# Kernel tuning notes

Hardware: AMD Instinct MI355X
Metric: run time of the kernel (lower is better)

## Reference

```python
import jax, jax.numpy as jnp
import numpy as np

N = 16      # degrees of freedom (state dim = 2N)
HID = 512   # MLP hidden width
B = 2048    # batch


def setup_inputs() -> dict:
    key = jax.random.key(0)
    ks = jax.random.split(key, 4)
    s = 0.05  # small init keeps the qd-qd Hessian block well conditioned
    return {
        "x": jax.random.normal(ks[0], (B, 2 * N), jnp.float32),
        "W1": jax.random.normal(ks[1], (2 * N, HID), jnp.float32) * s,
        "b1": jnp.zeros((HID,), jnp.float32),
        "W2": jax.random.normal(ks[2], (HID, HID), jnp.float32) * s,
        "b2": jnp.zeros((HID,), jnp.float32),
        "W3": jax.random.normal(ks[3], (HID, 1), jnp.float32) * s,
        "b3": jnp.zeros((1,), jnp.float32),
    }


def _lagrangian(qqd, W1, b1, W2, b2, W3, b3):
    # scalar Lagrangian L(q, qd) from a smooth MLP
    h = jax.nn.softplus(qqd @ W1 + b1)
    h = jax.nn.softplus(h @ W2 + b2)
    return (h @ W3 + b3)[0]


def reference(x, W1, b1, W2, b2, W3, b3):
    n = x.shape[1] // 2

    def dyn(qqd):  # qqd: [2n]
        lag = lambda z: _lagrangian(z, W1, b1, W2, b2, W3, b3)
        g = jax.grad(lag)(qqd)                 # J = dL/dqqd, [2n]
        H = jax.jacfwd(jax.grad(lag))(qqd)     # full Hessian, [2n, 2n]
        DL_q = g[:n]                           # dL/dq
        # T_k = sum_j qd_j * d2L/(dq_j dqd_k)  (mixed block)
        T = qqd[n:] @ H[:n, n:]
        Hinv = jnp.linalg.inv(H[n:, n:])       # [n, n], symmetric
        # torch einsum('ijk,ij->ik', inv, v) -> qdd_k = sum_j inv[j,k] v_j
        qdd = (DL_q - T) @ Hinv
        return jnp.concatenate([qqd[n:], qdd])  # [2n] = [qd, qdd]

    return jax.vmap(dyn)(x)
```

## Files before the change

kernel.cpp:

```cpp
#include <hip/hip_runtime.h>
#include <math.h>

#define HID 512
#define TW 32
#define NQ 16

#define SWZM(c) ((((c) + ((c) >> 2) + ((c) >> 4))) & 3)

#define RED6(v) { v += __shfl_xor(v, 32); v += __shfl_xor(v, 16); \
                  v += __shfl_xor(v, 8);  v += __shfl_xor(v, 4);  \
                  v += __shfl_xor(v, 2);  v += __shfl_xor(v, 1); }

__global__ __launch_bounds__(512) void k1_fwd(const float* __restrict__ x,
        const float* __restrict__ W1, const float* __restrict__ b1,
        float* __restrict__ s1g, float* __restrict__ h1g) {
    __shared__ float xr[TW];
    const int r = blockIdx.x;
    const int t = threadIdx.x;
    if (t < TW) xr[t] = x[r * TW + t];
    __syncthreads();
    float z = b1[t];
    #pragma unroll
    for (int k = 0; k < TW; ++k) z = fmaf(xr[k], W1[k * HID + t], z);
    float s = 1.f / (1.f + expf(-z));
    float h = fmaxf(z, 0.f) + log1pf(expf(-fabsf(z)));
    s1g[r * HID + t] = s;
    h1g[r * HID + t] = h;
}

__global__ __launch_bounds__(256) void k2_z2(const float* __restrict__ h1g,
        const float* __restrict__ W2, const float* __restrict__ b2,
        const float* __restrict__ W3,
        float* __restrict__ u2g, float* __restrict__ d2g) {
    __shared__ float As[16 * 36];
    __shared__ float Bs[16 * 64];
    const int tid = threadIdx.x;
    const int r0 = blockIdx.x * 32;
    const int n0 = blockIdx.y * 64;
    const int tm = tid >> 5;
    const int tn = tid & 31;
    float acc[4][2] = {};
    const int ar = tid >> 3;
    const int ak = (tid & 7) * 2;
    const int bk = tid >> 4;
    const int bn = (tid & 15) * 4;
    for (int k0 = 0; k0 < HID; k0 += 16) {
        __syncthreads();
        float2 av = *(const float2*)&h1g[(r0 + ar) * HID + k0 + ak];
        As[(ak + 0) * 36 + ar] = av.x;
        As[(ak + 1) * 36 + ar] = av.y;
        float4 bv = *(const float4*)&W2[(k0 + bk) * HID + n0 + bn];
        *(float4*)&Bs[bk * 64 + bn] = bv;
        __syncthreads();
        #pragma unroll
        for (int k = 0; k < 16; ++k) {
            float4 a4 = *(const float4*)&As[k * 36 + tm * 4];
            float2 bb = *(const float2*)&Bs[k * 64 + tn * 2];
            acc[0][0] = fmaf(a4.x, bb.x, acc[0][0]);
            acc[0][1] = fmaf(a4.x, bb.y, acc[0][1]);
            acc[1][0] = fmaf(a4.y, bb.x, acc[1][0]);
            acc[1][1] = fmaf(a4.y, bb.y, acc[1][1]);
            acc[2][0] = fmaf(a4.z, bb.x, acc[2][0]);
            acc[2][1] = fmaf(a4.z, bb.y, acc[2][1]);
            acc[3][0] = fmaf(a4.w, bb.x, acc[3][0]);
            acc[3][1] = fmaf(a4.w, bb.y, acc[3][1]);
        }
    }
    #pragma unroll
    for (int q = 0; q < 4; ++q) {
        #pragma unroll
        for (int p = 0; p < 2; ++p) {
            int rr = r0 + tm * 4 + q;
            int nn = n0 + tn * 2 + p;
            float z = acc[q][p] + b2[nn];
            float s = 1.f / (1.f + expf(-z));
            float w3v = W3[nn];
            u2g[rr * HID + nn] = s * w3v;
            d2g[rr * HID + nn] = s * (1.f - s) * w3v;
        }
    }
}

__global__ __launch_bounds__(256) void k3_v(const float* __restrict__ u2g,
        const float* __restrict__ W2, float* __restrict__ vg) {
    __shared__ float As[16 * 36];
    __shared__ float Bs[16 * 68];
    const int tid = threadIdx.x;
    const int r0 = blockIdx.x * 32;
    const int n0 = blockIdx.y * 64;
    const int tm = tid >> 5;
    const int tn = tid & 31;
    float acc[4][2] = {};
    const int ar = tid >> 3;
    const int ak = (tid & 7) * 2;
    const int ba = tid >> 2;
    const int bb0 = (tid & 3) * 4;
    for (int k0 = 0; k0 < HID; k0 += 16) {
        __syncthreads();
        float2 av = *(const float2*)&u2g[(r0 + ar) * HID + k0 + ak];
        As[(ak + 0) * 36 + ar] = av.x;
        As[(ak + 1) * 36 + ar] = av.y;
        float4 bv = *(const float4*)&W2[(n0 + ba) * HID + k0 + bb0];
        Bs[(bb0 + 0) * 68 + ba] = bv.x;
        Bs[(bb0 + 1) * 68 + ba] = bv.y;
        Bs[(bb0 + 2) * 68 + ba] = bv.z;
        Bs[(bb0 + 3) * 68 + ba] = bv.w;
        __syncthreads();
        #pragma unroll
        for (int k = 0; k < 16; ++k) {
            float4 a4 = *(const float4*)&As[k * 36 + tm * 4];
            float2 bb = *(const float2*)&Bs[k * 68 + tn * 2];
            acc[0][0] = fmaf(a4.x, bb.x, acc[0][0]);
            acc[0][1] = fmaf(a4.x, bb.y, acc[0][1]);
            acc[1][0] = fmaf(a4.y, bb.x, acc[1][0]);
            acc[1][1] = fmaf(a4.y, bb.y, acc[1][1]);
            acc[2][0] = fmaf(a4.z, bb.x, acc[2][0]);
            acc[2][1] = fmaf(a4.z, bb.y, acc[2][1]);
            acc[3][0] = fmaf(a4.w, bb.x, acc[3][0]);
            acc[3][1] = fmaf(a4.w, bb.y, acc[3][1]);
        }
    }
    #pragma unroll
    for (int q = 0; q < 4; ++q) {
        #pragma unroll
        for (int p = 0; p < 2; ++p) {
            vg[(r0 + tm * 4 + q) * HID + n0 + tn * 2 + p] = acc[q][p];
        }
    }
}

__global__ __launch_bounds__(512) void k2b_pack(const float* __restrict__ x,
        const float* __restrict__ W1, const float* __restrict__ s1g,
        float* __restrict__ s4g, float* __restrict__ u4g,
        float* __restrict__ wt2g) {
    __shared__ float qd[16];
    const int r = blockIdx.x;
    const int c = threadIdx.x;
    if (c < 16) qd[c] = x[r * TW + 16 + c];
    __syncthreads();
    float qw = 0.f;
    #pragma unroll
    for (int m = 0; m < 16; ++m) qw = fmaf(qd[m], W1[m * HID + c], qw);
    const float s = s1g[r * HID + c];
    const int base = (r >> 2) * 2048 + c * 4 + (r & 3);
    s4g[base] = s;
    u4g[base] = s * qw;
    if (r == 0) {
        #pragma unroll
        for (int j = 0; j < 16; ++j)
            wt2g[c * 16 + j] = W1[(16 + j) * HID + c];
    }
}

#define OFF_PT   0
#define OFF_W1T2 8192
#define OFF_WX   16384
#define OFF_YW   17408
#define OFF_H2B  18432
#define OFF_XR   19520
#define OFF_G16  19648
#define OFF_RSB  19712
#define OFF_MU   19776
#define OFF_QD   19840
#define OFF_PIV  19904
#define SMEM_FLOATS 19908

#define ACC16(rr, t)                                   \
  acc[rr][ 0]=fmaf(a0.x,t,acc[rr][ 0]);                \
  acc[rr][ 1]=fmaf(a0.y,t,acc[rr][ 1]);                \
  acc[rr][ 2]=fmaf(a0.z,t,acc[rr][ 2]);                \
  acc[rr][ 3]=fmaf(a0.w,t,acc[rr][ 3]);                \
  acc[rr][ 4]=fmaf(a1.x,t,acc[rr][ 4]);                \
  acc[rr][ 5]=fmaf(a1.y,t,acc[rr][ 5]);                \
  acc[rr][ 6]=fmaf(a1.z,t,acc[rr][ 6]);                \
  acc[rr][ 7]=fmaf(a1.w,t,acc[rr][ 7]);                \
  acc[rr][ 8]=fmaf(a2.x,t,acc[rr][ 8]);                \
  acc[rr][ 9]=fmaf(a2.y,t,acc[rr][ 9]);                \
  acc[rr][10]=fmaf(a2.z,t,acc[rr][10]);                \
  acc[rr][11]=fmaf(a2.w,t,acc[rr][11]);                \
  acc[rr][12]=fmaf(a3.x,t,acc[rr][12]);                \
  acc[rr][13]=fmaf(a3.y,t,acc[rr][13]);                \
  acc[rr][14]=fmaf(a3.z,t,acc[rr][14]);                \
  acc[rr][15]=fmaf(a3.w,t,acc[rr][15]);

__global__ __launch_bounds__(512, 2) void k4_main(
        const float* __restrict__ x, const float* __restrict__ W1,
        const float* __restrict__ W2,
        const float* __restrict__ s1g, const float* __restrict__ d2g,
        const float* __restrict__ vg,
        const float* __restrict__ s4g, const float* __restrict__ u4g,
        const float* __restrict__ wt2g,
        float* __restrict__ out) {
    __shared__ __align__(16) float sm[SMEM_FLOATS];
    const int tid = threadIdx.x;
    const int r0 = blockIdx.x * 4;
    float* PT   = sm + OFF_PT;
    float* W1T2 = sm + OFF_W1T2;
    float* WX   = sm + OFF_WX;
    float* YW   = sm + OFF_YW;
    float* H2B  = sm + OFF_H2B;
    float* XR   = sm + OFF_XR;
    float* G16  = sm + OFF_G16;
    float* RSB  = sm + OFF_RSB;
    float* MU   = sm + OFF_MU;
    float* QD   = sm + OFF_QD;
    int*   PIV  = (int*)(sm + OFF_PIV);

    const int w    = tid >> 6;
    const int lane = tid & 63;

    if (tid < 128) XR[tid] = x[(r0 + (tid >> 5)) * TW + (tid & 31)];
    {
        const int c = tid;
        const int m = SWZM(c);
        #pragma unroll
        for (int q = 0; q < 4; ++q) {
            float4 wv4;
            wv4.x = W1[(16 + q * 4 + 0) * HID + c];
            wv4.y = W1[(16 + q * 4 + 1) * HID + c];
            wv4.z = W1[(16 + q * 4 + 2) * HID + c];
            wv4.w = W1[(16 + q * 4 + 3) * HID + c];
            *(float4*)&W1T2[c * 16 + ((q ^ m) << 2)] = wv4;
        }
    }

    {
        const int rr1 = w >> 1;
        const int j0 = (w & 1) * 8;
        const float* srow = s1g + (size_t)(r0 + rr1) * HID;
        const float* vrow = vg + (size_t)(r0 + rr1) * HID;
        float gp[8];
        #pragma unroll
        for (int j = 0; j < 8; ++j) gp[j] = 0.f;
        #pragma unroll
        for (int it = 0; it < 8; ++it) {
            const int c = it * 64 + lane;
            const float sv = srow[c] * vrow[c];
            #pragma unroll
            for (int j = 0; j < 8; ++j)
                gp[j] = fmaf(W1[(j0 + j) * HID + c], sv, gp[j]);
        }
        #pragma unroll
        for (int j = 0; j < 8; ++j) { RED6(gp[j]); }
        if (lane == 0) {
            #pragma unroll
            for (int j = 0; j < 8; ++j) G16[rr1 * 16 + j0 + j] = gp[j];
        }
    }

    float acc[4][16];
    #pragma unroll
    for (int rr = 0; rr < 4; ++rr)
        #pragma unroll
        for (int i = 0; i < 16; ++i) acc[rr][i] = 0.f;
    float yv[4] = {0.f, 0.f, 0.f, 0.f};
    {
        const float4* wt4 = (const float4*)wt2g;
        const float4* s44 = (const float4*)s4g + (size_t)blockIdx.x * 512;
        const float4* u44 = (const float4*)u4g + (size_t)blockIdx.x * 512;
        const float* w2p = W2 + tid;
        #pragma unroll 1
        for (int c8 = 0; c8 < HID; c8 += 8) {
            float w2v[8];
            #pragma unroll
            for (int k = 0; k < 8; ++k) w2v[k] = w2p[(size_t)(c8 + k) * HID];
            #pragma unroll
            for (int k = 0; k < 8; ++k) {
                const int c = c8 + k;
                const float4 s4 = s44[c];
                const float4 u4 = u44[c];
                const float4 a0 = wt4[c * 4 + 0];
                const float4 a1 = wt4[c * 4 + 1];
                const float4 a2 = wt4[c * 4 + 2];
                const float4 a3 = wt4[c * 4 + 3];
                const float w2 = w2v[k];
                yv[0] = fmaf(u4.x, w2, yv[0]);
                yv[1] = fmaf(u4.y, w2, yv[1]);
                yv[2] = fmaf(u4.z, w2, yv[2]);
                yv[3] = fmaf(u4.w, w2, yv[3]);
                const float t0 = s4.x * w2;
                const float t1 = s4.y * w2;
                const float t2 = s4.z * w2;
                const float t3 = s4.w * w2;
                ACC16(0, t0)
                ACC16(1, t1)
                ACC16(2, t2)
                ACC16(3, t3)
            }
        }
    }

    const int i0 = 2 * w;
    const int qi = w >> 1;
    const bool hiH = (i0 & 3) == 2;
    #pragma unroll
    for (int rr = 0; rr < 4; ++rr) {
        __syncthreads();
        {
            const int c = tid;
            const float d2v = d2g[(size_t)(r0 + rr) * HID + c];
            const float vvv = vg[(size_t)(r0 + rr) * HID + c];
            const float s1v = s1g[(size_t)(r0 + rr) * HID + c];
            const float uv  = u4g[(size_t)blockIdx.x * 2048 + c * 4 + rr];
            WX[c] = d2v;
            WX[HID + c] = s1v * (1.f - s1v) * vvv;
            YW[c] = yv[rr] * d2v;
            YW[HID + c] = uv * (1.f - s1v) * vvv;
            const int m = SWZM(c);
            *(float4*)&PT[c * 16 + ((0 ^ m) << 2)] = make_float4(acc[rr][0], acc[rr][1], acc[rr][2], acc[rr][3]);
            *(float4*)&PT[c * 16 + ((1 ^ m) << 2)] = make_float4(acc[rr][4], acc[rr][5], acc[rr][6], acc[rr][7]);
            *(float4*)&PT[c * 16 + ((2 ^ m) << 2)] = make_float4(acc[rr][8], acc[rr][9], acc[rr][10], acc[rr][11]);
            *(float4*)&PT[c * 16 + ((3 ^ m) << 2)] = make_float4(acc[rr][12], acc[rr][13], acc[rr][14], acc[rr][15]);
        }
        __syncthreads();
        float hp0[16], hp1[16];
        #pragma unroll
        for (int e = 0; e < 16; ++e) { hp0[e] = 0.f; hp1[e] = 0.f; }
        float tp0 = 0.f, tp1 = 0.f;
        #pragma unroll
        for (int it = 0; it < 16; ++it) {
            const int b = (it & 7) * 64 + lane;
            const float* SRC = (it < 8) ? PT : W1T2;
            const float wv = (it < 8) ? WX[b] : WX[HID + b];
            const float yw = (it < 8) ? YW[b] : YW[HID + b];
            const int m = SWZM(b);
            const float4 eqi = *(const float4*)&SRC[b * 16 + ((qi ^ m) << 2)];
            const float Li0 = hiH ? eqi.z : eqi.x;
            const float Li1 = hiH ? eqi.w : eqi.y;
            const float a0v = Li0 * wv;
            const float a1v = Li1 * wv;
            tp0 = fmaf(yw, Li0, tp0);
            tp1 = fmaf(yw, Li1, tp1);
            const float4 e0 = *(const float4*)&SRC[b * 16 + ((0 ^ m) << 2)];
            hp0[0] = fmaf(a0v, e0.x, hp0[0]); hp0[1] = fmaf(a0v, e0.y, hp0[1]);
            hp0[2] = fmaf(a0v, e0.z, hp0[2]); hp0[3] = fmaf(a0v, e0.w, hp0[3]);
            hp1[0] = fmaf(a1v, e0.x, hp1[0]); hp1[1] = fmaf(a1v, e0.y, hp1[1]);
            hp1[2] = fmaf(a1v, e0.z, hp1[2]); hp1[3] = fmaf(a1v, e0.w, hp1[3]);
            const float4 e1 = *(const float4*)&SRC[b * 16 + ((1 ^ m) << 2)];
            hp0[4] = fmaf(a0v, e1.x, hp0[4]); hp0[5] = fmaf(a0v, e1.y, hp0[5]);
            hp0[6] = fmaf(a0v, e1.z, hp0[6]); hp0[7] = fmaf(a0v, e1.w, hp0[7]);
            hp1[4] = fmaf(a1v, e1.x, hp1[4]); hp1[5] = fmaf(a1v, e1.y, hp1[5]);
            hp1[6] = fmaf(a1v, e1.z, hp1[6]); hp1[7] = fmaf(a1v, e1.w, hp1[7]);
            const float4 e2 = *(const float4*)&SRC[b * 16 + ((2 ^ m) << 2)];
            hp0[8] = fmaf(a0v, e2.x, hp0[8]); hp0[9] = fmaf(a0v, e2.y, hp0[9]);
            hp0[10] = fmaf(a0v, e2.z, hp0[10]); hp0[11] = fmaf(a0v, e2.w, hp0[11]);
            hp1[8] = fmaf(a1v, e2.x, hp1[8]); hp1[9] = fmaf(a1v, e2.y, hp1[9]);
            hp1[10] = fmaf(a1v, e2.z, hp1[10]); hp1[11] = fmaf(a1v, e2.w, hp1[11]);
            const float4 e3 = *(const float4*)&SRC[b * 16 + ((3 ^ m) << 2)];
            hp0[12] = fmaf(a0v, e3.x, hp0[12]); hp0[13] = fmaf(a0v, e3.y, hp0[13]);
            hp0[14] = fmaf(a0v, e3.z, hp0[14]); hp0[15] = fmaf(a0v, e3.w, hp0[15]);
            hp1[12] = fmaf(a1v, e3.x, hp1[12]); hp1[13] = fmaf(a1v, e3.y, hp1[13]);
            hp1[14] = fmaf(a1v, e3.z, hp1[14]); hp1[15] = fmaf(a1v, e3.w, hp1[15]);
        }
        #pragma unroll
        for (int e = 0; e < 16; ++e) { RED6(hp0[e]); RED6(hp1[e]); }
        RED6(tp0); RED6(tp1);
        if (lane == 0) {
            float* H0 = H2B + rr * 272 + i0 * 17;
            #pragma unroll
            for (int e = 0; e < 16; ++e) { H0[e] = hp0[e]; H0[17 + e] = hp1[e]; }
            RSB[rr * 16 + i0]     = G16[rr * 16 + i0]     - tp0;
            RSB[rr * 16 + i0 + 1] = G16[rr * 16 + i0 + 1] - tp1;
        }
    }
    __syncthreads();

    {
        const int row = tid >> 7;
        const int lt = tid & 127;
        float* A = H2B + row * 272;
        float* rs = RSB + row * 16;
        for (int k = 0; k < 16; ++k) {
            if (lt == 0) {
                int p = k; float best = fabsf(A[k * 17 + k]);
                for (int r2 = k + 1; r2 < 16; ++r2) {
                    float v2 = fabsf(A[r2 * 17 + k]);
                    if (v2 > best) { best = v2; p = r2; }
                }
                PIV[row] = p;
            }
            __syncthreads();
            const int p = PIV[row];
            if (p != k) {
                if (lt < 16) {
                    float t1 = A[k * 17 + lt]; A[k * 17 + lt] = A[p * 17 + lt]; A[p * 17 + lt] = t1;
                } else if (lt == 16) {
                    float t1 = rs[k]; rs[k] = rs[p]; rs[p] = t1;
                }
            }
            __syncthreads();
            if (lt > k && lt < 16) MU[row * 16 + lt] = A[lt * 17 + k] / A[k * 17 + k];
            __syncthreads();
            {
                const int i2 = lt >> 3;
                const int j2 = (lt & 7) * 2;
                if (i2 > k) {
                    float mu = MU[row * 16 + i2];
                    A[i2 * 17 + j2]     = fmaf(-mu, A[k * 17 + j2],     A[i2 * 17 + j2]);
                    A[i2 * 17 + j2 + 1] = fmaf(-mu, A[k * 17 + j2 + 1], A[i2 * 17 + j2 + 1]);
                    if ((lt & 7) == 0) rs[i2] = fmaf(-mu, rs[k], rs[i2]);
                }
            }
            __syncthreads();
        }
        for (int k = 15; k >= 0; --k) {
            if (lt == 0) QD[row * 16 + k] = rs[k] / A[k * 17 + k];
            __syncthreads();
            if (lt < k) rs[lt] = fmaf(-QD[row * 16 + k], A[lt * 17 + k], rs[lt]);
            __syncthreads();
        }
    }

    if (tid < 128) {
        const int row = tid >> 5;
        const int e = tid & 31;
        out[(r0 + row) * TW + e] = (e < 16) ? XR[row * TW + 16 + e] : QD[row * 16 + e - 16];
    }
}

extern "C" void kernel_launch(void* const* d_in, const int* in_sizes, int n_in,
                              void* d_out, int out_size, void* d_ws, size_t ws_size,
                              hipStream_t stream) {
    const float* x  = (const float*)d_in[0];
    const float* W1 = (const float*)d_in[1];
    const float* b1 = (const float*)d_in[2];
    const float* W2 = (const float*)d_in[3];
    const float* b2 = (const float*)d_in[4];
    const float* W3 = (const float*)d_in[5];
    float* out = (float*)d_out;
    float* ws = (float*)d_ws;

    float* s1g  = ws;
    float* h1g  = ws + (1u << 20);
    float* u2g  = ws + 2u * (1u << 20);
    float* d2g  = ws + 3u * (1u << 20);
    float* vg   = ws + 4u * (1u << 20);
    float* wt2g = ws + 5u * (1u << 20);
    float* s4g  = h1g;
    float* u4g  = u2g;

    k1_fwd<<<2048, 512, 0, stream>>>(x, W1, b1, s1g, h1g);
    dim3 g2(64, 8);
    k2_z2<<<g2, 256, 0, stream>>>(h1g, W2, b2, W3, u2g, d2g);
    k3_v<<<g2, 256, 0, stream>>>(u2g, W2, vg);
    k2b_pack<<<2048, 512, 0, stream>>>(x, W1, s1g, s4g, u4g, wt2g);
    k4_main<<<512, 512, 0, stream>>>(x, W1, W2, s1g, d2g, vg, s4g, u4g, wt2g, out);
}
```

Measured before the change: 400.1 us.

## Process two batch rows per block in main kernel instead of four

The main Hessian kernel now handles two samples per block instead of four, doubling the grid to 1024 blocks. The packed s/u layout changes from groups of four rows to pairs, and the accumulator and shared-memory arrays shrink to match. Each LU solve now gets 256 threads, one matrix element per thread, and skips columns at or left of the pivot. The goal is more blocks to fill the GPU and fewer registers per thread. The cost is that W2 and the W1 tiles are reloaded twice as often across the grid, since each load is reused for fewer rows.

```diff
diff --git a/kernel.cpp b/kernel.cpp
--- a/kernel.cpp
+++ b/kernel.cpp
@@ -131,7 +131,7 @@
 
 __global__ __launch_bounds__(512) void k2b_pack(const float* __restrict__ x,
         const float* __restrict__ W1, const float* __restrict__ s1g,
-        float* __restrict__ s4g, float* __restrict__ u4g,
+        float* __restrict__ s2pk, float* __restrict__ u2pk,
         float* __restrict__ wt2g) {
     __shared__ float qd[16];
     const int r = blockIdx.x;
@@ -142,9 +142,9 @@
     #pragma unroll
     for (int m = 0; m < 16; ++m) qw = fmaf(qd[m], W1[m * HID + c], qw);
     const float s = s1g[r * HID + c];
-    const int base = (r >> 2) * 2048 + c * 4 + (r & 3);
-    s4g[base] = s;
-    u4g[base] = s * qw;
+    const int base = (r >> 1) * 1024 + c * 2 + (r & 1);
+    s2pk[base] = s;
+    u2pk[base] = s * qw;
     if (r == 0) {
         #pragma unroll
         for (int j = 0; j < 16; ++j)
@@ -157,13 +157,13 @@
 #define OFF_WX   16384
 #define OFF_YW   17408
 #define OFF_H2B  18432
-#define OFF_XR   19520
-#define OFF_G16  19648
-#define OFF_RSB  19712
-#define OFF_MU   19776
-#define OFF_QD   19840
-#define OFF_PIV  19904
-#define SMEM_FLOATS 19908
+#define OFF_XR   18976
+#define OFF_G16  19040
+#define OFF_RSB  19072
+#define OFF_MU   19104
+#define OFF_QD   19136
+#define OFF_PIV  19168
+#define SMEM_FLOATS 19172
 
 #define ACC16(rr, t)                                   \
   acc[rr][ 0]=fmaf(a0.x,t,acc[rr][ 0]);                \
@@ -188,12 +188,12 @@
         const float* __restrict__ W2,
         const float* __restrict__ s1g, const float* __restrict__ d2g,
         const float* __restrict__ vg,
-        const float* __restrict__ s4g, const float* __restrict__ u4g,
+        const float* __restrict__ s2pk, const float* __restrict__ u2pk,
         const float* __restrict__ wt2g,
         float* __restrict__ out) {
     __shared__ __align__(16) float sm[SMEM_FLOATS];
     const int tid = threadIdx.x;
-    const int r0 = blockIdx.x * 4;
+    const int r0 = blockIdx.x * 2;
     float* PT   = sm + OFF_PT;
     float* W1T2 = sm + OFF_W1T2;
     float* WX   = sm + OFF_WX;
@@ -209,7 +209,7 @@
     const int w    = tid >> 6;
     const int lane = tid & 63;
 
-    if (tid < 128) XR[tid] = x[(r0 + (tid >> 5)) * TW + (tid & 31)];
+    if (tid < 64) XR[tid] = x[(r0 + (tid >> 5)) * TW + (tid & 31)];
     {
         const int c = tid;
         const int m = SWZM(c);
@@ -225,39 +225,37 @@
     }
 
     {
-        const int rr1 = w >> 1;
-        const int j0 = (w & 1) * 8;
+        const int rr1 = w >> 2;
+        const int j0 = (w & 3) * 4;
         const float* srow = s1g + (size_t)(r0 + rr1) * HID;
         const float* vrow = vg + (size_t)(r0 + rr1) * HID;
-        float gp[8];
-        #pragma unroll
-        for (int j = 0; j < 8; ++j) gp[j] = 0.f;
+        float gp[4] = {0.f, 0.f, 0.f, 0.f};
         #pragma unroll
         for (int it = 0; it < 8; ++it) {
             const int c = it * 64 + lane;
             const float sv = srow[c] * vrow[c];
             #pragma unroll
-            for (int j = 0; j < 8; ++j)
+            for (int j = 0; j < 4; ++j)
                 gp[j] = fmaf(W1[(j0 + j) * HID + c], sv, gp[j]);
         }
         #pragma unroll
-        for (int j = 0; j < 8; ++j) { RED6(gp[j]); }
+        for (int j = 0; j < 4; ++j) { RED6(gp[j]); }
         if (lane == 0) {
             #pragma unroll
-            for (int j = 0; j < 8; ++j) G16[rr1 * 16 + j0 + j] = gp[j];
-        }
-    }
-
-    float acc[4][16];
-    #pragma unroll
-    for (int rr = 0; rr < 4; ++rr)
+            for (int j = 0; j < 4; ++j) G16[rr1 * 16 + j0 + j] = gp[j];
+        }
+    }
+
+    float acc[2][16];
+    #pragma unroll
+    for (int rr = 0; rr < 2; ++rr)
         #pragma unroll
         for (int i = 0; i < 16; ++i) acc[rr][i] = 0.f;
-    float yv[4] = {0.f, 0.f, 0.f, 0.f};
+    float yv[2] = {0.f, 0.f};
     {
         const float4* wt4 = (const float4*)wt2g;
-        const float4* s44 = (const float4*)s4g + (size_t)blockIdx.x * 512;
-        const float4* u44 = (const float4*)u4g + (size_t)blockIdx.x * 512;
+        const float2* s22 = (const float2*)s2pk + (size_t)blockIdx.x * 512;
+        const float2* u22 = (const float2*)u2pk + (size_t)blockIdx.x * 512;
         const float* w2p = W2 + tid;
         #pragma unroll 1
         for (int c8 = 0; c8 < HID; c8 += 8) {
@@ -267,25 +265,19 @@
             #pragma unroll
             for (int k = 0; k < 8; ++k) {
                 const int c = c8 + k;
-                const float4 s4 = s44[c];
-                const float4 u4 = u44[c];
+                const float2 s2 = s22[c];
+                const float2 u2 = u22[c];
                 const float4 a0 = wt4[c * 4 + 0];
                 const float4 a1 = wt4[c * 4 + 1];
                 const float4 a2 = wt4[c * 4 + 2];
                 const float4 a3 = wt4[c * 4 + 3];
                 const float w2 = w2v[k];
-                yv[0] = fmaf(u4.x, w2, yv[0]);
-                yv[1] = fmaf(u4.y, w2, yv[1]);
-                yv[2] = fmaf(u4.z, w2, yv[2]);
-                yv[3] = fmaf(u4.w, w2, yv[3]);
-                const float t0 = s4.x * w2;
-                const float t1 = s4.y * w2;
-                const float t2 = s4.z * w2;
-                const float t3 = s4.w * w2;
+                yv[0] = fmaf(u2.x, w2, yv[0]);
+                yv[1] = fmaf(u2.y, w2, yv[1]);
+                const float t0 = s2.x * w2;
+                const float t1 = s2.y * w2;
                 ACC16(0, t0)
                 ACC16(1, t1)
-                ACC16(2, t2)
-                ACC16(3, t3)
             }
         }
     }
@@ -294,14 +286,14 @@
     const int qi = w >> 1;
     const bool hiH = (i0 & 3) == 2;
     #pragma unroll
-    for (int rr = 0; rr < 4; ++rr) {
+    for (int rr = 0; rr < 2; ++rr) {
         __syncthreads();
         {
             const int c = tid;
             const float d2v = d2g[(size_t)(r0 + rr) * HID + c];
             const float vvv = vg[(size_t)(r0 + rr) * HID + c];
             const float s1v = s1g[(size_t)(r0 + rr) * HID + c];
-            const float uv  = u4g[(size_t)blockIdx.x * 2048 + c * 4 + rr];
+            const float uv  = u2pk[(size_t)blockIdx.x * 1024 + c * 2 + rr];
             WX[c] = d2v;
             WX[HID + c] = s1v * (1.f - s1v) * vvv;
             YW[c] = yv[rr] * d2v;
@@ -366,8 +358,8 @@
     __syncthreads();
 
     {
-        const int row = tid >> 7;
-        const int lt = tid & 127;
+        const int row = tid >> 8;
+        const int lt = tid & 255;
         float* A = H2B + row * 272;
         float* rs = RSB + row * 16;
         for (int k = 0; k < 16; ++k) {
@@ -392,13 +384,12 @@
             if (lt > k && lt < 16) MU[row * 16 + lt] = A[lt * 17 + k] / A[k * 17 + k];
             __syncthreads();
             {
-                const int i2 = lt >> 3;
-                const int j2 = (lt & 7) * 2;
+                const int i2 = lt >> 4;
+                const int j2 = lt & 15;
                 if (i2 > k) {
                     float mu = MU[row * 16 + i2];
-                    A[i2 * 17 + j2]     = fmaf(-mu, A[k * 17 + j2],     A[i2 * 17 + j2]);
-                    A[i2 * 17 + j2 + 1] = fmaf(-mu, A[k * 17 + j2 + 1], A[i2 * 17 + j2 + 1]);
-                    if ((lt & 7) == 0) rs[i2] = fmaf(-mu, rs[k], rs[i2]);
+                    if (j2 > k) A[i2 * 17 + j2] = fmaf(-mu, A[k * 17 + j2], A[i2 * 17 + j2]);
+                    if (j2 == 0) rs[i2] = fmaf(-mu, rs[k], rs[i2]);
                 }
             }
             __syncthreads();
@@ -411,7 +402,7 @@
         }
     }
 
-    if (tid < 128) {
+    if (tid < 64) {
         const int row = tid >> 5;
         const int e = tid & 31;
         out[(r0 + row) * TW + e] = (e < 16) ? XR[row * TW + 16 + e] : QD[row * 16 + e - 16];
@@ -436,13 +427,13 @@
     float* d2g  = ws + 3u * (1u << 20);
     float* vg   = ws + 4u * (1u << 20);
     float* wt2g = ws + 5u * (1u << 20);
-    float* s4g  = h1g;
-    float* u4g  = u2g;
+    float* s2pk = h1g;
+    float* u2pk = u2g;
 
     k1_fwd<<<2048, 512, 0, stream>>>(x, W1, b1, s1g, h1g);
     dim3 g2(64, 8);
     k2_z2<<<g2, 256, 0, stream>>>(h1g, W2, b2, W3, u2g, d2g);
     k3_v<<<g2, 256, 0, stream>>>(u2g, W2, vg);
-    k2b_pack<<<2048, 512, 0, stream>>>(x, W1, s1g, s4g, u4g, wt2g);
-    k4_main<<<512, 512, 0, stream>>>(x, W1, W2, s1g, d2g, vg, s4g, u4g, wt2g, out);
-}
+    k2b_pack<<<2048, 512, 0, stream>>>(x, W1, s1g, s2pk, u2pk, wt2g);
+    k4_main<<<1024, 512, 0, stream>>>(x, W1, W2, s1g, d2g, vg, s2pk, u2pk, wt2g, out);
+}
```

Result: slower. 443.7 us (+10.9%).

## Stage s/u and W1 qd-columns in LDS for main loop; split Hessian rows per wave

Applied to the files above, without the earlier changes.

The main accumulation loop in k4_main now reads the packed s/u values and the transposed W1 qd-columns from shared memory instead of global/L2, with the s/u block staged once into the PT region and held in registers for the later per-row phase. The global wt2g transposed copy and its producer in k2b_pack are removed. The Hessian-block assembly is reorganised so each wave computes one row at a time over two passes rather than two rows at once, reducing register pressure. The cost is an extra block-wide barrier and more LDS traffic in the hot loop.

```diff
diff --git a/kernel.cpp b/kernel.cpp
--- a/kernel.cpp
+++ b/kernel.cpp
@@ -131,8 +131,7 @@
 
 __global__ __launch_bounds__(512) void k2b_pack(const float* __restrict__ x,
         const float* __restrict__ W1, const float* __restrict__ s1g,
-        float* __restrict__ s4g, float* __restrict__ u4g,
-        float* __restrict__ wt2g) {
+        float* __restrict__ s4g, float* __restrict__ u4g) {
     __shared__ float qd[16];
     const int r = blockIdx.x;
     const int c = threadIdx.x;
@@ -145,11 +144,6 @@
     const int base = (r >> 2) * 2048 + c * 4 + (r & 3);
     s4g[base] = s;
     u4g[base] = s * qw;
-    if (r == 0) {
-        #pragma unroll
-        for (int j = 0; j < 16; ++j)
-            wt2g[c * 16 + j] = W1[(16 + j) * HID + c];
-    }
 }
 
 #define OFF_PT   0
@@ -183,18 +177,43 @@
   acc[rr][14]=fmaf(a3.z,t,acc[rr][14]);                \
   acc[rr][15]=fmaf(a3.w,t,acc[rr][15]);
 
+#define PH5_ROW(SRC, WXOFF, YWOFF, QI)                                       \
+  _Pragma("unroll 4")                                                        \
+  for (int it = 0; it < 8; ++it) {                                           \
+      const int b = it * 64 + lane;                                          \
+      const float wv = WX[WXOFF + b];                                        \
+      const float yw = YW[YWOFF + b];                                        \
+      const int m = SWZM(b);                                                 \
+      const float4 eqi = *(const float4*)&SRC[b * 16 + (((QI) ^ m) << 2)];   \
+      const float Li = c2 ? (c1 ? eqi.w : eqi.z) : (c1 ? eqi.y : eqi.x);     \
+      const float av = Li * wv;                                              \
+      tp = fmaf(yw, Li, tp);                                                 \
+      const float4 e0 = *(const float4*)&SRC[b * 16 + ((0 ^ m) << 2)];       \
+      hp[0] = fmaf(av, e0.x, hp[0]);   hp[1] = fmaf(av, e0.y, hp[1]);        \
+      hp[2] = fmaf(av, e0.z, hp[2]);   hp[3] = fmaf(av, e0.w, hp[3]);        \
+      const float4 e1 = *(const float4*)&SRC[b * 16 + ((1 ^ m) << 2)];       \
+      hp[4] = fmaf(av, e1.x, hp[4]);   hp[5] = fmaf(av, e1.y, hp[5]);        \
+      hp[6] = fmaf(av, e1.z, hp[6]);   hp[7] = fmaf(av, e1.w, hp[7]);        \
+      const float4 e2 = *(const float4*)&SRC[b * 16 + ((2 ^ m) << 2)];       \
+      hp[8] = fmaf(av, e2.x, hp[8]);   hp[9] = fmaf(av, e2.y, hp[9]);        \
+      hp[10] = fmaf(av, e2.z, hp[10]); hp[11] = fmaf(av, e2.w, hp[11]);      \
+      const float4 e3 = *(const float4*)&SRC[b * 16 + ((3 ^ m) << 2)];       \
+      hp[12] = fmaf(av, e3.x, hp[12]); hp[13] = fmaf(av, e3.y, hp[13]);      \
+      hp[14] = fmaf(av, e3.z, hp[14]); hp[15] = fmaf(av, e3.w, hp[15]);      \
+  }
+
 __global__ __launch_bounds__(512, 2) void k4_main(
         const float* __restrict__ x, const float* __restrict__ W1,
         const float* __restrict__ W2,
         const float* __restrict__ s1g, const float* __restrict__ d2g,
         const float* __restrict__ vg,
         const float* __restrict__ s4g, const float* __restrict__ u4g,
-        const float* __restrict__ wt2g,
         float* __restrict__ out) {
     __shared__ __align__(16) float sm[SMEM_FLOATS];
     const int tid = threadIdx.x;
     const int r0 = blockIdx.x * 4;
     float* PT   = sm + OFF_PT;
+    float* SU   = sm + OFF_PT;
     float* W1T2 = sm + OFF_W1T2;
     float* WX   = sm + OFF_WX;
     float* YW   = sm + OFF_YW;
@@ -210,6 +229,7 @@
     const int lane = tid & 63;
 
     if (tid < 128) XR[tid] = x[(r0 + (tid >> 5)) * TW + (tid & 31)];
+    float s1v0, s1v1, s1v2, s1v3, uv0, uv1, uv2, uv3;
     {
         const int c = tid;
         const int m = SWZM(c);
@@ -222,6 +242,12 @@
             wv4.w = W1[(16 + q * 4 + 3) * HID + c];
             *(float4*)&W1T2[c * 16 + ((q ^ m) << 2)] = wv4;
         }
+        const float4 s4 = ((const float4*)s4g)[(size_t)blockIdx.x * 512 + c];
+        const float4 u4 = ((const float4*)u4g)[(size_t)blockIdx.x * 512 + c];
+        s1v0 = s4.x; s1v1 = s4.y; s1v2 = s4.z; s1v3 = s4.w;
+        uv0 = u4.x; uv1 = u4.y; uv2 = u4.z; uv3 = u4.w;
+        *(float4*)&SU[c * 8] = s4;
+        *(float4*)&SU[c * 8 + 4] = u4;
     }
 
     {
@@ -247,6 +273,7 @@
             for (int j = 0; j < 8; ++j) G16[rr1 * 16 + j0 + j] = gp[j];
         }
     }
+    __syncthreads();
 
     float acc[4][16];
     #pragma unroll
@@ -255,9 +282,6 @@
         for (int i = 0; i < 16; ++i) acc[rr][i] = 0.f;
     float yv[4] = {0.f, 0.f, 0.f, 0.f};
     {
-        const float4* wt4 = (const float4*)wt2g;
-        const float4* s44 = (const float4*)s4g + (size_t)blockIdx.x * 512;
-        const float4* u44 = (const float4*)u4g + (size_t)blockIdx.x * 512;
         const float* w2p = W2 + tid;
         #pragma unroll 1
         for (int c8 = 0; c8 < HID; c8 += 8) {
@@ -267,21 +291,22 @@
             #pragma unroll
             for (int k = 0; k < 8; ++k) {
                 const int c = c8 + k;
-                const float4 s4 = s44[c];
-                const float4 u4 = u44[c];
-                const float4 a0 = wt4[c * 4 + 0];
-                const float4 a1 = wt4[c * 4 + 1];
-                const float4 a2 = wt4[c * 4 + 2];
-                const float4 a3 = wt4[c * 4 + 3];
+                const int m = SWZM(c);
+                const float4 su_s = *(const float4*)&SU[c * 8];
+                const float4 su_u = *(const float4*)&SU[c * 8 + 4];
+                const float4 a0 = *(const float4*)&W1T2[c * 16 + ((0 ^ m) << 2)];
+                const float4 a1 = *(const float4*)&W1T2[c * 16 + ((1 ^ m) << 2)];
+                const float4 a2 = *(const float4*)&W1T2[c * 16 + ((2 ^ m) << 2)];
+                const float4 a3 = *(const float4*)&W1T2[c * 16 + ((3 ^ m) << 2)];
                 const float w2 = w2v[k];
-                yv[0] = fmaf(u4.x, w2, yv[0]);
-                yv[1] = fmaf(u4.y, w2, yv[1]);
-                yv[2] = fmaf(u4.z, w2, yv[2]);
-                yv[3] = fmaf(u4.w, w2, yv[3]);
-                const float t0 = s4.x * w2;
-                const float t1 = s4.y * w2;
-                const float t2 = s4.z * w2;
-                const float t3 = s4.w * w2;
+                yv[0] = fmaf(su_u.x, w2, yv[0]);
+                yv[1] = fmaf(su_u.y, w2, yv[1]);
+                yv[2] = fmaf(su_u.z, w2, yv[2]);
+                yv[3] = fmaf(su_u.w, w2, yv[3]);
+                const float t0 = su_s.x * w2;
+                const float t1 = su_s.y * w2;
+                const float t2 = su_s.z * w2;
+                const float t3 = su_s.w * w2;
                 ACC16(0, t0)
                 ACC16(1, t1)
                 ACC16(2, t2)
@@ -290,9 +315,10 @@
         }
     }
 
-    const int i0 = 2 * w;
-    const int qi = w >> 1;
-    const bool hiH = (i0 & 3) == 2;
+    const int comp = w & 3;
+    const bool c1 = (comp & 1) != 0;
+    const bool c2 = (comp & 2) != 0;
+    const int qlo = w >> 2;
     #pragma unroll
     for (int rr = 0; rr < 4; ++rr) {
         __syncthreads();
@@ -300,8 +326,8 @@
             const int c = tid;
             const float d2v = d2g[(size_t)(r0 + rr) * HID + c];
             const float vvv = vg[(size_t)(r0 + rr) * HID + c];
-            const float s1v = s1g[(size_t)(r0 + rr) * HID + c];
-            const float uv  = u4g[(size_t)blockIdx.x * 2048 + c * 4 + rr];
+            const float s1v = (rr == 0) ? s1v0 : (rr == 1) ? s1v1 : (rr == 2) ? s1v2 : s1v3;
+            const float uv  = (rr == 0) ? uv0  : (rr == 1) ? uv1  : (rr == 2) ? uv2  : uv3;
             WX[c] = d2v;
             WX[HID + c] = s1v * (1.f - s1v) * vvv;
             YW[c] = yv[rr] * d2v;
@@ -313,54 +339,25 @@
             *(float4*)&PT[c * 16 + ((3 ^ m) << 2)] = make_float4(acc[rr][12], acc[rr][13], acc[rr][14], acc[rr][15]);
         }
         __syncthreads();
-        float hp0[16], hp1[16];
-        #pragma unroll
-        for (int e = 0; e < 16; ++e) { hp0[e] = 0.f; hp1[e] = 0.f; }
-        float tp0 = 0.f, tp1 = 0.f;
-        #pragma unroll
-        for (int it = 0; it < 16; ++it) {
-            const int b = (it & 7) * 64 + lane;
-            const float* SRC = (it < 8) ? PT : W1T2;
-            const float wv = (it < 8) ? WX[b] : WX[HID + b];
-            const float yw = (it < 8) ? YW[b] : YW[HID + b];
-            const int m = SWZM(b);
-            const float4 eqi = *(const float4*)&SRC[b * 16 + ((qi ^ m) << 2)];
-            const float Li0 = hiH ? eqi.z : eqi.x;
-            const float Li1 = hiH ? eqi.w : eqi.y;
-            const float a0v = Li0 * wv;
-            const float a1v = Li1 * wv;
-            tp0 = fmaf(yw, Li0, tp0);
-            tp1 = fmaf(yw, Li1, tp1);
-            const float4 e0 = *(const float4*)&SRC[b * 16 + ((0 ^ m) << 2)];
-            hp0[0] = fmaf(a0v, e0.x, hp0[0]); hp0[1] = fmaf(a0v, e0.y, hp0[1]);
-            hp0[2] = fmaf(a0v, e0.z, hp0[2]); hp0[3] = fmaf(a0v, e0.w, hp0[3]);
-            hp1[0] = fmaf(a1v, e0.x, hp1[0]); hp1[1] = fmaf(a1v, e0.y, hp1[1]);
-            hp1[2] = fmaf(a1v, e0.z, hp1[2]); hp1[3] = fmaf(a1v, e0.w, hp1[3]);
-            const float4 e1 = *(const float4*)&SRC[b * 16 + ((1 ^ m) << 2)];
-            hp0[4] = fmaf(a0v, e1.x, hp0[4]); hp0[5] = fmaf(a0v, e1.y, hp0[5]);
-            hp0[6] = fmaf(a0v, e1.z, hp0[6]); hp0[7] = fmaf(a0v, e1.w, hp0[7]);
-            hp1[4] = fmaf(a1v, e1.x, hp1[4]); hp1[5] = fmaf(a1v, e1.y, hp1[5]);
-            hp1[6] = fmaf(a1v, e1.z, hp1[6]); hp1[7] = fmaf(a1v, e1.w, hp1[7]);
-            const float4 e2 = *(const float4*)&SRC[b * 16 + ((2 ^ m) << 2)];
-            hp0[8] = fmaf(a0v, e2.x, hp0[8]); hp0[9] = fmaf(a0v, e2.y, hp0[9]);
-            hp0[10] = fmaf(a0v, e2.z, hp0[10]); hp0[11] = fmaf(a0v, e2.w, hp0[11]);
-            hp1[8] = fmaf(a1v, e2.x, hp1[8]); hp1[9] = fmaf(a1v, e2.y, hp1[9]);
-            hp1[10] = fmaf(a1v, e2.z, hp1[10]); hp1[11] = fmaf(a1v, e2.w, hp1[11]);
-            const float4 e3 = *(const float4*)&SRC[b * 16 + ((3 ^ m) << 2)];
-            hp0[12] = fmaf(a0v, e3.x, hp0[12]); hp0[13] = fmaf(a0v, e3.y, hp0[13]);
-            hp0[14] = fmaf(a0v, e3.z, hp0[14]); hp0[15] = fmaf(a0v, e3.w, hp0[15]);
-            hp1[12] = fmaf(a1v, e3.x, hp1[12]); hp1[13] = fmaf(a1v, e3.y, hp1[13]);
-            hp1[14] = fmaf(a1v, e3.z, hp1[14]); hp1[15] = fmaf(a1v, e3.w, hp1[15]);
-        }
-        #pragma unroll
-        for (int e = 0; e < 16; ++e) { RED6(hp0[e]); RED6(hp1[e]); }
-        RED6(tp0); RED6(tp1);
-        if (lane == 0) {
-            float* H0 = H2B + rr * 272 + i0 * 17;
-            #pragma unroll
-            for (int e = 0; e < 16; ++e) { H0[e] = hp0[e]; H0[17 + e] = hp1[e]; }
-            RSB[rr * 16 + i0]     = G16[rr * 16 + i0]     - tp0;
-            RSB[rr * 16 + i0 + 1] = G16[rr * 16 + i0 + 1] - tp1;
+        #pragma unroll
+        for (int h = 0; h < 2; ++h) {
+            const int i0 = 8 * h + w;
+            const int qi = 2 * h + qlo;
+            float hp[16];
+            #pragma unroll
+            for (int e = 0; e < 16; ++e) hp[e] = 0.f;
+            float tp = 0.f;
+            PH5_ROW(PT, 0, 0, qi)
+            PH5_ROW(W1T2, HID, HID, qi)
+            #pragma unroll
+            for (int e = 0; e < 16; ++e) { RED6(hp[e]); }
+            RED6(tp);
+            if (lane == 0) {
+                float* H0 = H2B + rr * 272 + i0 * 17;
+                #pragma unroll
+                for (int e = 0; e < 16; ++e) H0[e] = hp[e];
+                RSB[rr * 16 + i0] = G16[rr * 16 + i0] - tp;
+            }
         }
     }
     __syncthreads();
@@ -430,19 +427,18 @@
     float* out = (float*)d_out;
     float* ws = (float*)d_ws;
 
-    float* s1g  = ws;
-    float* h1g  = ws + (1u << 20);
-    float* u2g  = ws + 2u * (1u << 20);
-    float* d2g  = ws + 3u * (1u << 20);
-    float* vg   = ws + 4u * (1u << 20);
-    float* wt2g = ws + 5u * (1u << 20);
-    float* s4g  = h1g;
-    float* u4g  = u2g;
+    float* s1g = ws;
+    float* h1g = ws + (1u << 20);
+    float* u2g = ws + 2u * (1u << 20);
+    float* d2g = ws + 3u * (1u << 20);
+    float* vg  = ws + 4u * (1u << 20);
+    float* s4g = h1g;
+    float* u4g = u2g;
 
     k1_fwd<<<2048, 512, 0, stream>>>(x, W1, b1, s1g, h1g);
     dim3 g2(64, 8);
     k2_z2<<<g2, 256, 0, stream>>>(h1g, W2, b2, W3, u2g, d2g);
     k3_v<<<g2, 256, 0, stream>>>(u2g, W2, vg);
-    k2b_pack<<<2048, 512, 0, stream>>>(x, W1, s1g, s4g, u4g, wt2g);
-    k4_main<<<512, 512, 0, stream>>>(x, W1, W2, s1g, d2g, vg, s4g, u4g, wt2g, out);
-}
+    k2b_pack<<<2048, 512, 0, stream>>>(x, W1, s1g, s4g, u4g);
+    k4_main<<<512, 512, 0, stream>>>(x, W1, W2, s1g, d2g, vg, s4g, u4g, out);
+}
```

New measurement: 417.4 us. +4.3%, slower.
